# Kernel optimization log

Hardware: AMD Instinct MI355X
Metric: run time of the kernel (lower is better)

## Reference

```python
import jax, jax.numpy as jnp
import numpy as np

B, H, V, E, TOPK = 65536, 768, 512, 8, 2
D = H + V  # combined_dim = 1280


def setup_inputs() -> dict:
    key = jax.random.key(0)
    ks = jax.random.split(key, 12)
    def rn(k, sh, scale):
        return jax.random.normal(k, sh, dtype=jnp.float32) * scale
    return {
        "text_features": rn(ks[0], (B, H), 1.0),
        "video_features": rn(ks[1], (B, V), 1.0),
        # 8 stacked experts: 1280->256->128->1
        "exp_w1": rn(ks[2], (E, D, 256), 0.02), "exp_b1": jnp.zeros((E, 256), jnp.float32),
        "exp_w2": rn(ks[3], (E, 256, 128), 0.05), "exp_b2": jnp.zeros((E, 128), jnp.float32),
        "exp_w3": rn(ks[4], (E, 128, 1), 0.08), "exp_b3": jnp.zeros((E, 1), jnp.float32),
        # text router: 768->256->8
        "txt_r_w1": rn(ks[5], (H, 256), 0.03), "txt_r_b1": jnp.zeros((256,), jnp.float32),
        "txt_r_w2": rn(ks[6], (256, E), 0.06), "txt_r_b2": jnp.zeros((E,), jnp.float32),
        # video router: 512->256->8
        "vid_r_w1": rn(ks[7], (V, 256), 0.04), "vid_r_b1": jnp.zeros((256,), jnp.float32),
        "vid_r_w2": rn(ks[8], (256, E), 0.06), "vid_r_b2": jnp.zeros((E,), jnp.float32),
    }


def _router(x, w1, b1, w2, b2):
    return jax.nn.relu(x @ w1 + b1) @ w2 + b2  # [B, E]


def _aggregate(expert_outs, idx, weights):
    # expert_outs: [B, E]; idx/weights: [B, TOPK]
    chosen = jnp.take_along_axis(expert_outs, idx, axis=1)  # [B, TOPK]
    return jnp.sum(weights * chosen, axis=-1, keepdims=True)  # [B, 1]


def reference(text_features, video_features,
              exp_w1, exp_b1, exp_w2, exp_b2, exp_w3, exp_b3,
              txt_r_w1, txt_r_b1, txt_r_w2, txt_r_b2,
              vid_r_w1, vid_r_b1, vid_r_w2, vid_r_b2):
    combined = jnp.concatenate([text_features, video_features], axis=-1)  # [B, D]

    t_logits = _router(text_features, txt_r_w1, txt_r_b1, txt_r_w2, txt_r_b2)
    v_logits = _router(video_features, vid_r_w1, vid_r_b1, vid_r_w2, vid_r_b2)

    t_val, t_idx = jax.lax.top_k(t_logits, TOPK)
    v_val, v_idx = jax.lax.top_k(v_logits, TOPK)
    t_w = jax.nn.softmax(t_val, axis=-1)
    v_w = jax.nn.softmax(v_val, axis=-1)

    # Dense evaluation of all 8 experts (matches original Python loop, vectorized)
    h1 = jax.nn.relu(jnp.einsum('bd,edh->beh', combined, exp_w1) + exp_b1)  # [B,E,256]
    h2 = jax.nn.relu(jnp.einsum('beh,ehf->bef', h1, exp_w2) + exp_b2)       # [B,E,128]
    eo = jax.nn.sigmoid(jnp.einsum('bef,efo->beo', h2, exp_w3) + exp_b3)    # [B,E,1]
    eo = eo[:, :, 0]  # [B, E]

    text_conf = _aggregate(eo, t_idx, t_w)   # [B, 1]
    video_conf = _aggregate(eo, v_idx, v_w)  # [B, 1]
    return text_conf, video_conf
```

## Files before the change

### kernel.cpp

```cpp
#include <hip/hip_runtime.h>
#include <stdint.h>
#include <math.h>

#define B_N 65536
#define H_N 768
#define V_N 512
#define D_N 1280
#define E_N 8
#define N1  256
#define N2  128

#define W1E (E_N*D_N*N1)
#define W2E (E_N*N1*N2)
#define TRE (24*16*512)
#define VRE (16*16*512)

#define DELTA    5e-3f
#define FLAG_CAP 8192

typedef __attribute__((ext_vector_type(8))) short bf16x8;
typedef __attribute__((ext_vector_type(4))) float f32x4;

__device__ __forceinline__ unsigned short f2bf(float f){
  union{float f;uint32_t u;}v; v.f=f;
  uint32_t r = v.u + 0x7FFFu + ((v.u>>16)&1u);
  return (unsigned short)(r>>16);
}
__device__ __forceinline__ float bf2f(unsigned short s){
  union{uint32_t u; float f;}v; v.u = ((uint32_t)s)<<16; return v.f;
}

__global__ void convert_weights(const float* __restrict__ w1,
                                const float* __restrict__ w2,
                                const float* __restrict__ tw1,
                                const float* __restrict__ vw1,
                                unsigned short* __restrict__ w1b,
                                unsigned short* __restrict__ w2b,
                                unsigned short* __restrict__ t_hi,
                                unsigned short* __restrict__ t_lo,
                                unsigned short* __restrict__ v_hi,
                                unsigned short* __restrict__ v_lo,
                                int* __restrict__ counters){
  int i = blockIdx.x*256 + threadIdx.x;
  if (i < 16) counters[i] = 0;
  if (i < W1E){
    int tile = i >> 9, r = i & 511;
    int l = r >> 3, j = r & 7;
    int gt = tile & 15, t2 = tile >> 4;
    int ks = t2 % 40, e = t2 / 40;
    int k = ks*32 + 8*(l>>4) + j;
    int n = gt*16 + (l&15);
    w1b[i] = f2bf(w1[((size_t)e*D_N + k)*N1 + n]);
    return;
  }
  i -= W1E;
  if (i < W2E){
    int tile = i >> 9, r = i & 511;
    int l = r >> 3, j = r & 7;
    int ft = tile & 7, t2 = tile >> 3;
    int ks = t2 & 7, e = t2 >> 3;
    int k = ks*32 + 8*(l>>4) + j;
    int f = ft*16 + (l&15);
    w2b[i] = f2bf(w2[((size_t)e*N1 + k)*N2 + f]);
    return;
  }
  i -= W2E;
  if (i < TRE){
    int tile = i >> 9, r = i & 511;
    int l = r >> 3, j = r & 7;
    int gt = tile & 15, ks = tile >> 4;
    int k = ks*32 + 8*(l>>4) + j;
    int n = gt*16 + (l&15);
    float x = tw1[(size_t)k*N1 + n];
    unsigned short h = f2bf(x);
    t_hi[i] = h;
    t_lo[i] = f2bf(x - bf2f(h));
    return;
  }
  i -= TRE;
  if (i < VRE){
    int tile = i >> 9, r = i & 511;
    int l = r >> 3, j = r & 7;
    int gt = tile & 15, ks = tile >> 4;
    int k = ks*32 + 8*(l>>4) + j;
    int n = gt*16 + (l&15);
    float x = vw1[(size_t)k*N1 + n];
    unsigned short h = f2bf(x);
    v_hi[i] = h;
    v_lo[i] = f2bf(x - bf2f(h));
  }
}

__global__ __launch_bounds__(512,4) void router_mfma(
    const float* __restrict__ text, const float* __restrict__ video,
    const unsigned short* __restrict__ t_hi, const unsigned short* __restrict__ t_lo,
    const unsigned short* __restrict__ v_hi, const unsigned short* __restrict__ v_lo,
    const float* __restrict__ tb1, const float* __restrict__ tw2, const float* __restrict__ tb2,
    const float* __restrict__ vb1, const float* __restrict__ vw2, const float* __restrict__ vb2,
    int* __restrict__ selIdx, float2* __restrict__ selW,
    int* __restrict__ flags, int* __restrict__ counters,
    unsigned short* __restrict__ comb, int writeComb)
{
  __shared__ union {
    unsigned short a[4*2560];
    float h[64*264];
  } s;
  __shared__ float W2s[256*8];

  const int tid = threadIdx.x;
  const int rt = blockIdx.x >> 10;
  const int r0 = (blockIdx.x & 1023) * 64;
  const float* X = rt ? video : text;
  const unsigned short* Whi = rt ? v_hi : t_hi;
  const unsigned short* Wlo = rt ? v_lo : t_lo;
  const float* b1 = rt ? vb1 : tb1;
  const float* W2 = rt ? vw2 : tw2;
  const float* b2 = rt ? vb2 : tb2;
  const int K  = rt ? V_N : H_N;
  const int NK = K >> 5;
  const int cbase = rt ? H_N : 0;

  const int w = tid >> 6, l = tid & 63;
  const int mw = w & 1, nw = w >> 1;
  const int srow = tid >> 3, skq = (tid & 7) * 4;

  for (int i = tid; i < 2048; i += 512) W2s[i] = W2[i];

  f32x4 acc[2][4];
#pragma unroll
  for (int a=0;a<2;a++)
#pragma unroll
    for (int b=0;b<4;b++) acc[a][b] = (f32x4){0.f,0.f,0.f,0.f};

  const float* xrow = X + (size_t)(r0 + srow)*K + skq;
  float4 areg = *(const float4*)xrow;

  for (int ks = 0; ks < NK; ++ks){
    {
      unsigned short* dhi = s.a + (ks&1)*2560 + srow*40 + skq;
      unsigned short* dlo = s.a + (2+(ks&1))*2560 + srow*40 + skq;
      ushort4 uh, ul;
      uh.x = f2bf(areg.x); ul.x = f2bf(areg.x - bf2f(uh.x));
      uh.y = f2bf(areg.y); ul.y = f2bf(areg.y - bf2f(uh.y));
      uh.z = f2bf(areg.z); ul.z = f2bf(areg.z - bf2f(uh.z));
      uh.w = f2bf(areg.w); ul.w = f2bf(areg.w - bf2f(uh.w));
      *(ushort4*)dhi = uh;
      *(ushort4*)dlo = ul;
      if (writeComb)
        *(ushort4*)(comb + (size_t)(r0+srow)*D_N + cbase + ks*32 + skq) = uh;
    }
    if (ks + 1 < NK) areg = *(const float4*)(xrow + (ks+1)*32);
    __syncthreads();

    bf16x8 bh[4], bl[4];
#pragma unroll
    for (int nt=0;nt<4;nt++){
      size_t off = (size_t)(ks*16 + nw*4 + nt)*512 + l*8;
      bh[nt] = *(const bf16x8*)(Whi + off);
      bl[nt] = *(const bf16x8*)(Wlo + off);
    }
    bf16x8 ah[2], al[2];
    const unsigned short* ahi = s.a + (ks&1)*2560;
    const unsigned short* alo = s.a + (2+(ks&1))*2560;
#pragma unroll
    for (int mt=0;mt<2;mt++){
      int ro = (mw*32 + mt*16 + (l&15))*40 + 8*(l>>4);
      ah[mt] = *(const bf16x8*)(ahi + ro);
      al[mt] = *(const bf16x8*)(alo + ro);
    }
#pragma unroll
    for (int mt=0;mt<2;mt++)
#pragma unroll
      for (int nt=0;nt<4;nt++){
        acc[mt][nt] = __builtin_amdgcn_mfma_f32_16x16x32_bf16(ah[mt], bh[nt], acc[mt][nt], 0,0,0);
        acc[mt][nt] = __builtin_amdgcn_mfma_f32_16x16x32_bf16(ah[mt], bl[nt], acc[mt][nt], 0,0,0);
        acc[mt][nt] = __builtin_amdgcn_mfma_f32_16x16x32_bf16(al[mt], bh[nt], acc[mt][nt], 0,0,0);
      }
  }
  __syncthreads();

#pragma unroll
  for (int mt=0;mt<2;mt++){
#pragma unroll
    for (int nt=0;nt<4;nt++){
      int n = nw*64 + nt*16 + (l&15);
      float b1v = b1[n];
#pragma unroll
      for (int i=0;i<4;i++){
        int row = mw*32 + mt*16 + (l>>4)*4 + i;
        float v = acc[mt][nt][i] + b1v;
        s.h[row*264 + n] = v > 0.f ? v : 0.f;
      }
    }
  }
  __syncthreads();

  {
    const int r = tid >> 3, j = tid & 7;
    float part[8];
#pragma unroll
    for (int e=0;e<8;e++) part[e] = 0.f;
    for (int q=0;q<32;q++){
      int n = j + 8*q;
      float hv = s.h[r*264 + n];
#pragma unroll
      for (int e=0;e<8;e++) part[e] += hv * W2s[n*8 + e];
    }
#pragma unroll
    for (int m=1;m<=4;m<<=1)
#pragma unroll
      for (int e=0;e<8;e++) part[e] += __shfl_xor(part[e], m);

    if (j == 0){
      int row = r0 + r;
      float L[8];
#pragma unroll
      for (int e=0;e<8;e++) L[e] = part[e] + b2[e];
      int i0 = 0; float v0 = L[0];
#pragma unroll
      for (int e=1;e<8;e++) if (L[e] > v0){ v0 = L[e]; i0 = e; }
      int i1 = -1; float v1 = -1e30f;
#pragma unroll
      for (int e=0;e<8;e++) if (e != i0 && L[e] > v1){ v1 = L[e]; i1 = e; }
      float v2 = -1e30f;
#pragma unroll
      for (int e=0;e<8;e++) if (e != i0 && e != i1 && L[e] > v2) v2 = L[e];
      if (v1 - v2 < DELTA){
        int idx = atomicAdd(&counters[0], 1);
        if (idx < FLAG_CAP) flags[idx] = (rt<<16) | row;
      }
      float e1 = expf(v1 - v0);
      float invd = 1.f/(1.f + e1);
      selIdx[rt*B_N + row] = i0 | (i1 << 8);
      selW[rt*B_N + row] = make_float2(invd, e1*invd);
    }
  }
}

__global__ __launch_bounds__(256) void router_exact(
    const float* __restrict__ text, const float* __restrict__ video,
    const float* __restrict__ tw1, const float* __restrict__ tb1,
    const float* __restrict__ tw2, const float* __restrict__ tb2,
    const float* __restrict__ vw1, const float* __restrict__ vb1,
    const float* __restrict__ vw2, const float* __restrict__ vb2,
    int* __restrict__ selIdx, float2* __restrict__ selW,
    const int* __restrict__ flags, const int* __restrict__ counters)
{
  int nf = counters[0]; if (nf > FLAG_CAP) nf = FLAG_CAP;
  if ((int)blockIdx.x >= nf) return;
  int code = flags[blockIdx.x];
  int rt = code >> 16, row = code & 0xFFFF;
  const float* X  = rt ? video : text;
  const float* W1 = rt ? vw1 : tw1;
  const float* b1 = rt ? vb1 : tb1;
  const float* W2 = rt ? vw2 : tw2;
  const float* b2 = rt ? vb2 : tb2;
  const int K = rt ? V_N : H_N;

  __shared__ float xs[H_N];
  __shared__ double red[4][8];
  const int tid = threadIdx.x;
  for (int k = tid; k < K; k += 256) xs[k] = X[(size_t)row*K + k];
  __syncthreads();

  double sAcc = 0.0;
  for (int k = 0; k < K; ++k)
    sAcc += (double)xs[k] * (double)W1[(size_t)k*N1 + tid];
  sAcc += (double)b1[tid];
  double h = sAcc > 0.0 ? sAcc : 0.0;

  double p[8];
#pragma unroll
  for (int e=0;e<8;e++) p[e] = h * (double)W2[tid*8 + e];
#pragma unroll
  for (int m=1;m<=32;m<<=1)
#pragma unroll
    for (int e=0;e<8;e++) p[e] += __shfl_xor(p[e], m);
  if ((tid & 63) == 0){
#pragma unroll
    for (int e=0;e<8;e++) red[tid>>6][e] = p[e];
  }
  __syncthreads();
  if (tid == 0){
    double L[8];
#pragma unroll
    for (int e=0;e<8;e++) L[e] = red[0][e]+red[1][e]+red[2][e]+red[3][e] + (double)b2[e];
    int i0 = 0; double v0 = L[0];
#pragma unroll
    for (int e=1;e<8;e++) if (L[e] > v0){ v0 = L[e]; i0 = e; }
    int i1 = -1; double v1 = -1e300;
#pragma unroll
    for (int e=0;e<8;e++) if (e != i0 && L[e] > v1){ v1 = L[e]; i1 = e; }
    double e1 = exp(v1 - v0);
    double invd = 1.0/(1.0 + e1);
    selIdx[rt*B_N + row] = i0 | (i1 << 8);
    selW[rt*B_N + row] = make_float2((float)invd, (float)(e1*invd));
  }
}

__global__ __launch_bounds__(256) void bucket_build(
    const int* __restrict__ selIdx, int* __restrict__ bucket,
    int* __restrict__ counters)
{
  __shared__ int lcnt[8], lbase[8], lpos[8];
  const int tid = threadIdx.x;
  const int row = blockIdx.x*256 + tid;
  if (tid < 8){ lcnt[tid] = 0; lpos[tid] = 0; }
  __syncthreads();
  int st = selIdx[row], sv = selIdx[B_N + row];
  int mask = (1<<(st&7)) | (1<<((st>>8)&7)) | (1<<(sv&7)) | (1<<((sv>>8)&7));
#pragma unroll
  for (int e=0;e<8;e++) if ((mask>>e)&1) atomicAdd(&lcnt[e], 1);
  __syncthreads();
  if (tid < 8) lbase[tid] = atomicAdd(&counters[8+tid], lcnt[tid]);
  __syncthreads();
#pragma unroll
  for (int e=0;e<8;e++)
    if ((mask>>e)&1){
      int p = atomicAdd(&lpos[e], 1);
      bucket[e*B_N + lbase[e] + p] = row;
    }
}

template<int BF16A>
__global__ __launch_bounds__(512,4) void expert_sparse(
    const unsigned short* __restrict__ comb,
    const float* __restrict__ text, const float* __restrict__ video,
    const unsigned short* __restrict__ w1b, const float* __restrict__ b1,
    const unsigned short* __restrict__ w2b, const float* __restrict__ b2,
    const float* __restrict__ w3, const float* __restrict__ b3,
    const int* __restrict__ bucket, const int* __restrict__ counters,
    float* __restrict__ eo)
{
  __shared__ __align__(16) unsigned short As[4096];
  __shared__ __align__(16) unsigned short h1s[32768];
  __shared__ int rl[128];

  const int tid = threadIdx.x;
  const int e = blockIdx.x & 7;
  const int t = blockIdx.x >> 3;
  const int n_e = counters[8 + e];
  if (t*128 >= n_e) return;

  if (tid < 128){
    int idx = t*128 + tid;
    rl[tid] = (idx < n_e) ? bucket[e*B_N + idx] : -1;
  }
  __syncthreads();

  const int w = tid >> 6, l = tid & 63;
  const int mw = w & 1, nw = w >> 1;

  const int sridx = rl[(tid>>6)*16 + (l&15)];
  const int srr = sridx < 0 ? 0 : sridx;

  f32x4 acc[4][4];
#pragma unroll
  for (int a=0;a<4;a++)
#pragma unroll
    for (int b=0;b<4;b++) acc[a][b] = (f32x4){0.f,0.f,0.f,0.f};

  const unsigned short* w1e = w1b + (size_t)e*40*16*512;

  bf16x8 bfc[4];
#pragma unroll
  for (int nt=0;nt<4;nt++)
    bfc[nt] = *(const bf16x8*)(w1e + (size_t)(nw*4 + nt)*512 + l*8);

  if constexpr (BF16A){
    const unsigned short* arow = comb + (size_t)srr*D_N + (l>>4)*8;
    bf16x8 rc = *(const bf16x8*)arow;
    bf16x8 rn = *(const bf16x8*)(arow + 32);

    for (int ks = 0; ks < 40; ++ks){
      *(bf16x8*)(As + tid*8) = rc;
      rc = rn;
      if (ks + 2 < 40) rn = *(const bf16x8*)(arow + (ks+2)*32);
      __syncthreads();

      bf16x8 af[4];
#pragma unroll
      for (int mt=0;mt<4;mt++)
        af[mt] = *(const bf16x8*)(As + (mw*4+mt)*512 + l*8);

      bf16x8 bfn[4];
      if (ks + 1 < 40){
#pragma unroll
        for (int nt=0;nt<4;nt++)
          bfn[nt] = *(const bf16x8*)(w1e + (size_t)((ks+1)*16 + nw*4 + nt)*512 + l*8);
      }
#pragma unroll
      for (int mt=0;mt<4;mt++)
#pragma unroll
        for (int nt=0;nt<4;nt++)
          acc[mt][nt] = __builtin_amdgcn_mfma_f32_16x16x32_bf16(af[mt], bfc[nt], acc[mt][nt], 0,0,0);
      if (ks + 1 < 40){
#pragma unroll
        for (int nt=0;nt<4;nt++) bfc[nt] = bfn[nt];
      }
      __syncthreads();
    }
  } else {
    const float* tb = text  + (size_t)srr*H_N + (l>>4)*8;
    const float* vb = video + (size_t)srr*V_N + (l>>4)*8;
    float4 fa0 = *(const float4*)tb;
    float4 fa1 = *(const float4*)(tb + 4);

    for (int ks = 0; ks < 40; ++ks){
      {
        union { bf16x8 v; unsigned short u[8]; } sw;
        sw.u[0]=f2bf(fa0.x); sw.u[1]=f2bf(fa0.y); sw.u[2]=f2bf(fa0.z); sw.u[3]=f2bf(fa0.w);
        sw.u[4]=f2bf(fa1.x); sw.u[5]=f2bf(fa1.y); sw.u[6]=f2bf(fa1.z); sw.u[7]=f2bf(fa1.w);
        *(bf16x8*)(As + tid*8) = sw.v;
      }
      if (ks < 39){
        int k0 = (ks+1)*32;
        const float* p = (k0 < H_N) ? (tb + k0) : (vb + (k0 - H_N));
        fa0 = *(const float4*)p;
        fa1 = *(const float4*)(p + 4);
      }
      __syncthreads();

      bf16x8 af[4];
#pragma unroll
      for (int mt=0;mt<4;mt++)
        af[mt] = *(const bf16x8*)(As + (mw*4+mt)*512 + l*8);

      bf16x8 bfn[4];
      if (ks < 39){
#pragma unroll
        for (int nt=0;nt<4;nt++)
          bfn[nt] = *(const bf16x8*)(w1e + (size_t)((ks+1)*16 + nw*4 + nt)*512 + l*8);
      }
#pragma unroll
      for (int mt=0;mt<4;mt++)
#pragma unroll
        for (int nt=0;nt<4;nt++)
          acc[mt][nt] = __builtin_amdgcn_mfma_f32_16x16x32_bf16(af[mt], bfc[nt], acc[mt][nt], 0,0,0);
      if (ks < 39){
#pragma unroll
        for (int nt=0;nt<4;nt++) bfc[nt] = bfn[nt];
      }
      __syncthreads();
    }
  }

#pragma unroll
  for (int mt=0;mt<4;mt++){
#pragma unroll
    for (int nt=0;nt<4;nt++){
      int n = nw*64 + nt*16 + (l&15);
      float b1v = b1[e*N1 + n];
      int tile = (mw*4+mt)*8 + (n>>5);
      int sub  = 16*((n>>3)&3);
      int jj   = n & 7;
#pragma unroll
      for (int i=0;i<4;i++){
        int r15 = (l>>4)*4 + i;
        float v = acc[mt][nt][i] + b1v;
        v = v > 0.f ? v : 0.f;
        h1s[tile*512 + (r15 + sub)*8 + jj] = f2bf(v);
      }
    }
  }
  __syncthreads();

  f32x4 acc2[4][2];
#pragma unroll
  for (int a=0;a<4;a++)
#pragma unroll
    for (int b=0;b<2;b++) acc2[a][b] = (f32x4){0.f,0.f,0.f,0.f};
  const unsigned short* w2e = w2b + (size_t)e*8*8*512;
#pragma unroll
  for (int ks2=0; ks2<8; ++ks2){
    bf16x8 af2[4], bf2v[2];
#pragma unroll
    for (int mt=0;mt<4;mt++)
      af2[mt] = *(const bf16x8*)(h1s + ((mw*4+mt)*8 + ks2)*512 + l*8);
#pragma unroll
    for (int ft=0;ft<2;ft++)
      bf2v[ft] = *(const bf16x8*)(w2e + (size_t)(ks2*8 + nw*2 + ft)*512 + l*8);
#pragma unroll
    for (int mt=0;mt<4;mt++)
#pragma unroll
      for (int ft=0;ft<2;ft++)
        acc2[mt][ft] = __builtin_amdgcn_mfma_f32_16x16x32_bf16(af2[mt], bf2v[ft], acc2[mt][ft], 0,0,0);
  }

  {
    const float* w3e = w3 + e*N2;
    const float* b2e = b2 + e*N2;
    const int f0 = nw*32 + (l&15);
    const int f1 = f0 + 16;
    float w3v0 = w3e[f0], w3v1 = w3e[f1];
    float b2v0 = b2e[f0], b2v1 = b2e[f1];
    float* red = (float*)As;
#pragma unroll
    for (int mt=0;mt<4;mt++){
#pragma unroll
      for (int i=0;i<4;i++){
        float h20 = acc2[mt][0][i] + b2v0; h20 = h20 > 0.f ? h20 : 0.f;
        float h21 = acc2[mt][1][i] + b2v1; h21 = h21 > 0.f ? h21 : 0.f;
        float p = h20*w3v0 + h21*w3v1;
        p += __shfl_xor(p, 1);
        p += __shfl_xor(p, 2);
        p += __shfl_xor(p, 4);
        p += __shfl_xor(p, 8);
        if ((l & 15) == 0){
          int row = mw*64 + mt*16 + (l>>4)*4 + i;
          red[row*4 + nw] = p;
        }
      }
    }
    __syncthreads();
    if (tid < 128){
      int r = rl[tid];
      if (r >= 0){
        float sum = red[tid*4+0] + red[tid*4+1] + red[tid*4+2] + red[tid*4+3] + b3[e];
        eo[(size_t)r*E_N + e] = 1.f/(1.f + expf(-sum));
      }
    }
  }
}

__global__ __launch_bounds__(512) void aggregate_kernel(
    const int* __restrict__ selIdx, const float2* __restrict__ selW,
    const float* __restrict__ eo, float* __restrict__ out)
{
  int row = blockIdx.x*512 + threadIdx.x;
#pragma unroll
  for (int rt=0; rt<2; rt++){
    int s = selIdx[rt*B_N + row];
    float2 wv = selW[rt*B_N + row];
    out[(size_t)rt*B_N + row] = wv.x * eo[(size_t)row*E_N + (s&7)]
                              + wv.y * eo[(size_t)row*E_N + ((s>>8)&7)];
  }
}

extern "C" void kernel_launch(void* const* d_in, const int* in_sizes, int n_in,
                              void* d_out, int out_size, void* d_ws, size_t ws_size,
                              hipStream_t stream){
  const float* text   = (const float*)d_in[0];
  const float* video  = (const float*)d_in[1];
  const float* exp_w1 = (const float*)d_in[2];
  const float* exp_b1 = (const float*)d_in[3];
  const float* exp_w2 = (const float*)d_in[4];
  const float* exp_b2 = (const float*)d_in[5];
  const float* exp_w3 = (const float*)d_in[6];
  const float* exp_b3 = (const float*)d_in[7];
  const float* tw1 = (const float*)d_in[8];
  const float* tb1 = (const float*)d_in[9];
  const float* tw2 = (const float*)d_in[10];
  const float* tb2 = (const float*)d_in[11];
  const float* vw1 = (const float*)d_in[12];
  const float* vb1 = (const float*)d_in[13];
  const float* vw2 = (const float*)d_in[14];
  const float* vb2 = (const float*)d_in[15];
  float* out = (float*)d_out;

  size_t off = 0;
  auto alloc = [&](size_t bytes) -> char* {
    char* p = (char*)d_ws + off;
    off += (bytes + 255) & ~(size_t)255;
    return p;
  };
  int*    counters = (int*)   alloc(16*4);
  int*    flags    = (int*)   alloc((size_t)FLAG_CAP*4);
  int*    selIdx   = (int*)   alloc((size_t)2*B_N*4);
  float2* selW     = (float2*)alloc((size_t)2*B_N*8);
  int*    bucket   = (int*)   alloc((size_t)8*B_N*4);
  float*  eo       = (float*) alloc((size_t)B_N*E_N*4);
  unsigned short* w1b  = (unsigned short*)alloc((size_t)W1E*2);
  unsigned short* w2b  = (unsigned short*)alloc((size_t)W2E*2);
  unsigned short* t_hi = (unsigned short*)alloc((size_t)TRE*2);
  unsigned short* t_lo = (unsigned short*)alloc((size_t)TRE*2);
  unsigned short* v_hi = (unsigned short*)alloc((size_t)VRE*2);
  unsigned short* v_lo = (unsigned short*)alloc((size_t)VRE*2);
  unsigned short* comb = (unsigned short*)alloc((size_t)B_N*D_N*2);
  const int useComb = (off <= ws_size) ? 1 : 0;

  convert_weights<<<12544, 256, 0, stream>>>(exp_w1, exp_w2, tw1, vw1,
                                             w1b, w2b, t_hi, t_lo, v_hi, v_lo,
                                             counters);
  router_mfma<<<2048, 512, 0, stream>>>(text, video, t_hi, t_lo, v_hi, v_lo,
                                        tb1, tw2, tb2, vb1, vw2, vb2,
                                        selIdx, selW, flags, counters,
                                        comb, useComb);
  router_exact<<<FLAG_CAP, 256, 0, stream>>>(text, video, tw1, tb1, tw2, tb2,
                                             vw1, vb1, vw2, vb2,
                                             selIdx, selW, flags, counters);
  bucket_build<<<256, 256, 0, stream>>>(selIdx, bucket, counters);
  if (useComb){
    expert_sparse<1><<<4096, 512, 0, stream>>>(comb, text, video,
                                               w1b, exp_b1, w2b, exp_b2,
                                               exp_w3, exp_b3, bucket, counters, eo);
  } else {
    expert_sparse<0><<<4096, 512, 0, stream>>>(comb, text, video,
                                               w1b, exp_b1, w2b, exp_b2,
                                               exp_w3, exp_b3, bucket, counters, eo);
  }
  aggregate_kernel<<<128, 512, 0, stream>>>(selIdx, selW, eo, out);
}
```

Baseline: 574.5 us.

## Make expert buckets row-ordered and load A fragments directly from global memory

Bucket building now uses a count/scan/fill pass with warp ballots, so rows land in each expert bucket in a deterministic, ascending order instead of the order set by atomics. In the sparse expert kernel, the shared-memory staging of the A tile and its two barriers per k-step are removed. Each lane now reads its MFMA A fragments straight from the combined bf16 rows. This removes LDS traffic and synchronisation, but it adds two kernel launches and four times as many global A loads per thread, which rely on cache hits.

```diff
diff --git a/kernel.cpp b/kernel.cpp
--- a/kernel.cpp
+++ b/kernel.cpp
@@ -298,28 +298,74 @@
   }
 }
 
-__global__ __launch_bounds__(256) void bucket_build(
-    const int* __restrict__ selIdx, int* __restrict__ bucket,
-    int* __restrict__ counters)
+__device__ __forceinline__ int sel_mask(const int* selIdx, int row){
+  int st = selIdx[row], sv = selIdx[B_N + row];
+  return (1<<(st&7)) | (1<<((st>>8)&7)) | (1<<(sv&7)) | (1<<((sv>>8)&7));
+}
+
+__global__ __launch_bounds__(256) void bucket_count(
+    const int* __restrict__ selIdx, int* __restrict__ cnt)
 {
-  __shared__ int lcnt[8], lbase[8], lpos[8];
+  __shared__ int lcnt[8];
   const int tid = threadIdx.x;
+  if (tid < 8) lcnt[tid] = 0;
+  __syncthreads();
+  int mask = sel_mask(selIdx, blockIdx.x*256 + tid);
+#pragma unroll
+  for (int e=0;e<8;e++) if ((mask>>e)&1) atomicAdd(&lcnt[e], 1);
+  __syncthreads();
+  if (tid < 8) cnt[blockIdx.x*8 + tid] = lcnt[tid];
+}
+
+__global__ __launch_bounds__(256) void bucket_scan(
+    const int* __restrict__ cnt, int* __restrict__ base, int* __restrict__ counters)
+{
+  __shared__ int s[256];
+  const int tid = threadIdx.x;
+  for (int e=0;e<8;e++){
+    int v = cnt[tid*8 + e];
+    s[tid] = v; __syncthreads();
+    for (int o=1;o<256;o<<=1){
+      int t = (tid >= o) ? s[tid-o] : 0;
+      __syncthreads();
+      s[tid] += t;
+      __syncthreads();
+    }
+    base[tid*8 + e] = s[tid] - v;
+    if (tid == 255) counters[8+e] = s[255];
+    __syncthreads();
+  }
+}
+
+__global__ __launch_bounds__(256) void bucket_fill(
+    const int* __restrict__ selIdx, const int* __restrict__ base,
+    int* __restrict__ bucket)
+{
+  __shared__ int wtot[4][8], wexcl[4][8];
+  const int tid = threadIdx.x;
+  const int w = tid >> 6;
+  const unsigned long long lt = (1ULL << (tid & 63)) - 1ULL;
   const int row = blockIdx.x*256 + tid;
-  if (tid < 8){ lcnt[tid] = 0; lpos[tid] = 0; }
-  __syncthreads();
-  int st = selIdx[row], sv = selIdx[B_N + row];
-  int mask = (1<<(st&7)) | (1<<((st>>8)&7)) | (1<<(sv&7)) | (1<<((sv>>8)&7));
-#pragma unroll
-  for (int e=0;e<8;e++) if ((mask>>e)&1) atomicAdd(&lcnt[e], 1);
-  __syncthreads();
-  if (tid < 8) lbase[tid] = atomicAdd(&counters[8+tid], lcnt[tid]);
+  int mask = sel_mask(selIdx, row);
+  int rank[8];
+#pragma unroll
+  for (int e=0;e<8;e++){
+    unsigned long long b = __ballot((mask>>e)&1);
+    rank[e] = (int)__popcll(b & lt);
+    if ((tid & 63) == 0) wtot[w][e] = (int)__popcll(b);
+  }
+  __syncthreads();
+  if (tid < 32){
+    int e = tid & 7, ww = tid >> 3;
+    int sum = 0;
+    for (int x=0;x<ww;x++) sum += wtot[x][e];
+    wexcl[ww][e] = sum;
+  }
   __syncthreads();
 #pragma unroll
   for (int e=0;e<8;e++)
-    if ((mask>>e)&1){
-      int p = atomicAdd(&lpos[e], 1);
-      bucket[e*B_N + lbase[e] + p] = row;
-    }
+    if ((mask>>e)&1)
+      bucket[e*B_N + base[blockIdx.x*8 + e] + wexcl[w][e] + rank[e]] = row;
 }
 
 template<int BF16A>
@@ -351,9 +397,6 @@
   const int w = tid >> 6, l = tid & 63;
   const int mw = w & 1, nw = w >> 1;
 
-  const int sridx = rl[(tid>>6)*16 + (l&15)];
-  const int srr = sridx < 0 ? 0 : sridx;
-
   f32x4 acc[4][4];
 #pragma unroll
   for (int a=0;a<4;a++)
@@ -368,21 +411,18 @@
     bfc[nt] = *(const bf16x8*)(w1e + (size_t)(nw*4 + nt)*512 + l*8);
 
   if constexpr (BF16A){
-    const unsigned short* arow = comb + (size_t)srr*D_N + (l>>4)*8;
-    bf16x8 rc = *(const bf16x8*)arow;
-    bf16x8 rn = *(const bf16x8*)(arow + 32);
-
+    const unsigned short* ab[4];
+#pragma unroll
+    for (int mt=0;mt<4;mt++){
+      int rr = rl[(mw*4+mt)*16 + (l&15)];
+      if (rr < 0) rr = 0;
+      ab[mt] = comb + (size_t)rr*D_N + 8*(l>>4);
+    }
     for (int ks = 0; ks < 40; ++ks){
-      *(bf16x8*)(As + tid*8) = rc;
-      rc = rn;
-      if (ks + 2 < 40) rn = *(const bf16x8*)(arow + (ks+2)*32);
-      __syncthreads();
-
       bf16x8 af[4];
 #pragma unroll
       for (int mt=0;mt<4;mt++)
-        af[mt] = *(const bf16x8*)(As + (mw*4+mt)*512 + l*8);
-
+        af[mt] = *(const bf16x8*)(ab[mt] + ks*32);
       bf16x8 bfn[4];
       if (ks + 1 < 40){
 #pragma unroll
@@ -398,9 +438,10 @@
 #pragma unroll
         for (int nt=0;nt<4;nt++) bfc[nt] = bfn[nt];
       }
-      __syncthreads();
     }
   } else {
+    const int sridx = rl[(tid>>6)*16 + (l&15)];
+    const int srr = sridx < 0 ? 0 : sridx;
     const float* tb = text  + (size_t)srr*H_N + (l>>4)*8;
     const float* vb = video + (size_t)srr*V_N + (l>>4)*8;
     float4 fa0 = *(const float4*)tb;
@@ -569,6 +610,8 @@
   int*    selIdx   = (int*)   alloc((size_t)2*B_N*4);
   float2* selW     = (float2*)alloc((size_t)2*B_N*8);
   int*    bucket   = (int*)   alloc((size_t)8*B_N*4);
+  int*    cnt      = (int*)   alloc((size_t)256*8*4);
+  int*    base     = (int*)   alloc((size_t)256*8*4);
   float*  eo       = (float*) alloc((size_t)B_N*E_N*4);
   unsigned short* w1b  = (unsigned short*)alloc((size_t)W1E*2);
   unsigned short* w2b  = (unsigned short*)alloc((size_t)W2E*2);
@@ -589,7 +632,9 @@
   router_exact<<<FLAG_CAP, 256, 0, stream>>>(text, video, tw1, tb1, tw2, tb2,
                                              vw1, vb1, vw2, vb2,
                                              selIdx, selW, flags, counters);
-  bucket_build<<<256, 256, 0, stream>>>(selIdx, bucket, counters);
+  bucket_count<<<256, 256, 0, stream>>>(selIdx, cnt);
+  bucket_scan<<<1, 256, 0, stream>>>(cnt, base, counters);
+  bucket_fill<<<256, 256, 0, stream>>>(selIdx, base, bucket);
   if (useComb){
     expert_sparse<1><<<4096, 512, 0, stream>>>(comb, text, video,
                                                w1b, exp_b1, w2b, exp_b2,
```

Result: slower. 859.9 us (+49.7%).

## Stream expert tiles via global_load_lds double buffer and trim router split precision

Applied to the files above, without the earlier changes.

In the BF16 expert path, A rows and W1 tiles are now copied straight from global memory into double-buffered LDS with global_load_lds, in place of register-staged global loads and LDS stores. The A and h1 shared buffers are aliased to cut LDS use. The router drops the activation lo-part MFMA, going from 3 to 2 bf16 products, and the flag margin DELTA is doubled to absorb the extra error. The cost is lower router precision and possibly more rows flagged for fallback.

```diff
diff --git a/kernel.cpp b/kernel.cpp
--- a/kernel.cpp
+++ b/kernel.cpp
@@ -15,7 +15,7 @@
 #define TRE (24*16*512)
 #define VRE (16*16*512)
 
-#define DELTA    5e-3f
+#define DELTA    1e-2f
 #define FLAG_CAP 8192
 
 typedef __attribute__((ext_vector_type(8))) short bf16x8;
@@ -28,6 +28,11 @@
 }
 __device__ __forceinline__ float bf2f(unsigned short s){
   union{uint32_t u; float f;}v; v.u = ((uint32_t)s)<<16; return v.f;
+}
+__device__ __forceinline__ void glds16(const unsigned short* g, unsigned short* l){
+  __builtin_amdgcn_global_load_lds(
+      (const __attribute__((address_space(1))) void*)g,
+      (__attribute__((address_space(3))) void*)l, 16, 0, 0);
 }
 
 __global__ void convert_weights(const float* __restrict__ w1,
@@ -102,7 +107,7 @@
     unsigned short* __restrict__ comb, int writeComb)
 {
   __shared__ union {
-    unsigned short a[4*2560];
+    unsigned short a[2*2560];
     float h[64*264];
   } s;
   __shared__ float W2s[256*8];
@@ -138,14 +143,12 @@
   for (int ks = 0; ks < NK; ++ks){
     {
       unsigned short* dhi = s.a + (ks&1)*2560 + srow*40 + skq;
-      unsigned short* dlo = s.a + (2+(ks&1))*2560 + srow*40 + skq;
-      ushort4 uh, ul;
-      uh.x = f2bf(areg.x); ul.x = f2bf(areg.x - bf2f(uh.x));
-      uh.y = f2bf(areg.y); ul.y = f2bf(areg.y - bf2f(uh.y));
-      uh.z = f2bf(areg.z); ul.z = f2bf(areg.z - bf2f(uh.z));
-      uh.w = f2bf(areg.w); ul.w = f2bf(areg.w - bf2f(uh.w));
+      ushort4 uh;
+      uh.x = f2bf(areg.x);
+      uh.y = f2bf(areg.y);
+      uh.z = f2bf(areg.z);
+      uh.w = f2bf(areg.w);
       *(ushort4*)dhi = uh;
-      *(ushort4*)dlo = ul;
       if (writeComb)
         *(ushort4*)(comb + (size_t)(r0+srow)*D_N + cbase + ks*32 + skq) = uh;
     }
@@ -159,14 +162,12 @@
       bh[nt] = *(const bf16x8*)(Whi + off);
       bl[nt] = *(const bf16x8*)(Wlo + off);
     }
-    bf16x8 ah[2], al[2];
+    bf16x8 ah[2];
     const unsigned short* ahi = s.a + (ks&1)*2560;
-    const unsigned short* alo = s.a + (2+(ks&1))*2560;
 #pragma unroll
     for (int mt=0;mt<2;mt++){
       int ro = (mw*32 + mt*16 + (l&15))*40 + 8*(l>>4);
       ah[mt] = *(const bf16x8*)(ahi + ro);
-      al[mt] = *(const bf16x8*)(alo + ro);
     }
 #pragma unroll
     for (int mt=0;mt<2;mt++)
@@ -174,7 +175,6 @@
       for (int nt=0;nt<4;nt++){
         acc[mt][nt] = __builtin_amdgcn_mfma_f32_16x16x32_bf16(ah[mt], bh[nt], acc[mt][nt], 0,0,0);
         acc[mt][nt] = __builtin_amdgcn_mfma_f32_16x16x32_bf16(ah[mt], bl[nt], acc[mt][nt], 0,0,0);
-        acc[mt][nt] = __builtin_amdgcn_mfma_f32_16x16x32_bf16(al[mt], bh[nt], acc[mt][nt], 0,0,0);
       }
   }
   __syncthreads();
@@ -332,9 +332,11 @@
     const int* __restrict__ bucket, const int* __restrict__ counters,
     float* __restrict__ eo)
 {
-  __shared__ __align__(16) unsigned short As[4096];
-  __shared__ __align__(16) unsigned short h1s[32768];
+  __shared__ __align__(16) unsigned short shr[32768];
   __shared__ int rl[128];
+
+  unsigned short* As  = shr;
+  unsigned short* h1s = shr;
 
   const int tid = threadIdx.x;
   const int e = blockIdx.x & 7;
@@ -351,9 +353,6 @@
   const int w = tid >> 6, l = tid & 63;
   const int mw = w & 1, nw = w >> 1;
 
-  const int sridx = rl[(tid>>6)*16 + (l&15)];
-  const int srr = sridx < 0 ? 0 : sridx;
-
   f32x4 acc[4][4];
 #pragma unroll
   for (int a=0;a<4;a++)
@@ -362,49 +361,54 @@
 
   const unsigned short* w1e = w1b + (size_t)e*40*16*512;
 
-  bf16x8 bfc[4];
-#pragma unroll
-  for (int nt=0;nt<4;nt++)
-    bfc[nt] = *(const bf16x8*)(w1e + (size_t)(nw*4 + nt)*512 + l*8);
-
   if constexpr (BF16A){
-    const unsigned short* arow = comb + (size_t)srr*D_N + (l>>4)*8;
-    bf16x8 rc = *(const bf16x8*)arow;
-    bf16x8 rn = *(const bf16x8*)(arow + 32);
+    int rr = rl[w*16 + (l&15)]; if (rr < 0) rr = 0;
+    const unsigned short* gsA = comb + (size_t)rr*D_N + 8*(l>>4);
+
+    {
+      unsigned short* b0 = As;
+      glds16(gsA, b0 + w*512);
+      glds16(w1e + (size_t)(0*512 + w*64 + l)*8, b0 + 4096 + (0*512 + w*64)*8);
+      glds16(w1e + (size_t)(1*512 + w*64 + l)*8, b0 + 4096 + (1*512 + w*64)*8);
+    }
 
     for (int ks = 0; ks < 40; ++ks){
-      *(bf16x8*)(As + tid*8) = rc;
-      rc = rn;
-      if (ks + 2 < 40) rn = *(const bf16x8*)(arow + (ks+2)*32);
       __syncthreads();
-
-      bf16x8 af[4];
+      if (ks + 1 < 40){
+        unsigned short* nb = As + (((ks+1)&1) ? 12288 : 0);
+        const unsigned short* srcB = w1e + (size_t)(ks+1)*8192;
+        glds16(gsA + (ks+1)*32, nb + w*512);
+        glds16(srcB + (size_t)(0*512 + w*64 + l)*8, nb + 4096 + (0*512 + w*64)*8);
+        glds16(srcB + (size_t)(1*512 + w*64 + l)*8, nb + 4096 + (1*512 + w*64)*8);
+      }
+      const unsigned short* Acur = As + (ks&1)*12288;
+      const unsigned short* Bcur = Acur + 4096;
+      bf16x8 af[4], bf[4];
 #pragma unroll
       for (int mt=0;mt<4;mt++)
-        af[mt] = *(const bf16x8*)(As + (mw*4+mt)*512 + l*8);
-
-      bf16x8 bfn[4];
-      if (ks + 1 < 40){
+        af[mt] = *(const bf16x8*)(Acur + (mw*4+mt)*512 + l*8);
+#pragma unroll
+      for (int nt=0;nt<4;nt++)
+        bf[nt] = *(const bf16x8*)(Bcur + (nw*4+nt)*512 + l*8);
+#pragma unroll
+      for (int mt=0;mt<4;mt++)
 #pragma unroll
         for (int nt=0;nt<4;nt++)
-          bfn[nt] = *(const bf16x8*)(w1e + (size_t)((ks+1)*16 + nw*4 + nt)*512 + l*8);
-      }
-#pragma unroll
-      for (int mt=0;mt<4;mt++)
-#pragma unroll
-        for (int nt=0;nt<4;nt++)
-          acc[mt][nt] = __builtin_amdgcn_mfma_f32_16x16x32_bf16(af[mt], bfc[nt], acc[mt][nt], 0,0,0);
-      if (ks + 1 < 40){
-#pragma unroll
-        for (int nt=0;nt<4;nt++) bfc[nt] = bfn[nt];
-      }
-      __syncthreads();
-    }
+          acc[mt][nt] = __builtin_amdgcn_mfma_f32_16x16x32_bf16(af[mt], bf[nt], acc[mt][nt], 0,0,0);
+    }
+    __syncthreads();
   } else {
+    const int sridx = rl[(tid>>6)*16 + (l&15)];
+    const int srr = sridx < 0 ? 0 : sridx;
     const float* tb = text  + (size_t)srr*H_N + (l>>4)*8;
     const float* vb = video + (size_t)srr*V_N + (l>>4)*8;
     float4 fa0 = *(const float4*)tb;
     float4 fa1 = *(const float4*)(tb + 4);
+
+    bf16x8 bfc[4];
+#pragma unroll
+    for (int nt=0;nt<4;nt++)
+      bfc[nt] = *(const bf16x8*)(w1e + (size_t)(nw*4 + nt)*512 + l*8);
 
     for (int ks = 0; ks < 40; ++ks){
       {
@@ -486,6 +490,7 @@
       for (int ft=0;ft<2;ft++)
         acc2[mt][ft] = __builtin_amdgcn_mfma_f32_16x16x32_bf16(af2[mt], bf2v[ft], acc2[mt][ft], 0,0,0);
   }
+  __syncthreads();
 
   {
     const float* w3e = w3 + e*N2;
@@ -494,7 +499,7 @@
     const int f1 = f0 + 16;
     float w3v0 = w3e[f0], w3v1 = w3e[f1];
     float b2v0 = b2e[f0], b2v1 = b2e[f1];
-    float* red = (float*)As;
+    float* red = (float*)shr;
 #pragma unroll
     for (int mt=0;mt<4;mt++){
 #pragma unroll
```

New measurement: 635.7 us. 10.7% more time.
